# Optimization experiments

Measured on AMD Instinct MI355X. Metric: run time of the kernel, lower is better.

## Reference

```python
import jax, jax.numpy as jnp
import numpy as np

SEM_ENC_DIM = 1024
SENT_HIDDEN_DIM = 1024
ATT_DIM = 512

def setup_inputs() -> dict:
    key = jax.random.key(0)
    ks = jax.random.split(key, 8)
    B, L = 64, 2048
    s = lambda d: 1.0 / np.sqrt(d)
    return {
        "sem_enc_output": jax.random.normal(ks[0], (B, L, SEM_ENC_DIM), dtype=jnp.float32),
        "dec_hidden_state": jax.random.normal(ks[1], (B, SENT_HIDDEN_DIM), dtype=jnp.float32),
        "W_enc": jax.random.uniform(ks[2], (SEM_ENC_DIM, ATT_DIM), jnp.float32, -s(SEM_ENC_DIM), s(SEM_ENC_DIM)),
        "b_enc": jax.random.uniform(ks[3], (ATT_DIM,), jnp.float32, -s(SEM_ENC_DIM), s(SEM_ENC_DIM)),
        "W_dec": jax.random.uniform(ks[4], (SENT_HIDDEN_DIM, ATT_DIM), jnp.float32, -s(SENT_HIDDEN_DIM), s(SENT_HIDDEN_DIM)),
        "b_dec": jax.random.uniform(ks[5], (ATT_DIM,), jnp.float32, -s(SENT_HIDDEN_DIM), s(SENT_HIDDEN_DIM)),
        "W_full": jax.random.uniform(ks[6], (ATT_DIM, 1), jnp.float32, -s(ATT_DIM), s(ATT_DIM)),
        "b_full": jax.random.uniform(ks[7], (1,), jnp.float32, -s(ATT_DIM), s(ATT_DIM)),
    }

def reference(sem_enc_output, dec_hidden_state, W_enc, b_enc, W_dec, b_dec, W_full, b_full):
    # enc projection: [B, L, att_dim]
    enc_proj = jnp.einsum('ble,ea->bla', sem_enc_output, W_enc) + b_enc
    # dec projection: [B, att_dim]
    dec_proj = dec_hidden_state @ W_dec + b_dec
    # broadcast add + tanh: [B, L, att_dim]
    joined = jnp.tanh(enc_proj + dec_proj[:, None, :])
    # scoring: [B, L]
    scores = (jnp.einsum('bla,a->bl', joined, W_full[:, 0]) + b_full[0])
    att_scores = jax.nn.softmax(scores, axis=1)
    # weighted sum over L of the PROJECTED encoder output (matches torch code)
    att_output = jnp.einsum('bl,bla->ba', att_scores, enc_proj)
    return (att_output, att_scores)
```

## Files before the change

### kernel.cpp

```cpp
#include <hip/hip_runtime.h>
#include <hip/hip_bf16.h>
#include <cstdint>
#include <cstddef>

#define BB   64
#define LL   2048
#define ED   1024
#define AD   512
#define BM   64
#define NCH  (LL / BM)
#define KST  32

typedef short  short4v __attribute__((ext_vector_type(4)));
typedef short  short8  __attribute__((ext_vector_type(8)));
typedef float  f32x4   __attribute__((ext_vector_type(4)));

__device__ __forceinline__ unsigned short f2bf(float x) {
  unsigned u = __float_as_uint(x);
  u += 0x7FFFu + ((u >> 16) & 1u);
  return (unsigned short)(u >> 16);
}

__device__ __forceinline__ short4v cvt4(f32x4 v) {
  union { short4v s; unsigned u[2]; } r;
  asm("v_cvt_pk_bf16_f32 %0, %1, %2" : "=v"(r.u[0]) : "v"(v[0]), "v"(v[1]));
  asm("v_cvt_pk_bf16_f32 %0, %1, %2" : "=v"(r.u[1]) : "v"(v[2]), "v"(v[3]));
  return r.s;
}

#define GLOAD_LDS16(gp, lp)                                                        \
  __builtin_amdgcn_global_load_lds(                                                \
      (const __attribute__((address_space(1))) unsigned int*)(gp),                 \
      (__attribute__((address_space(3))) unsigned int*)(lp), 16, 0, 0)

__global__ __launch_bounds__(512) void prep_kernel(
    const float* __restrict__ W_enc, const float* __restrict__ dec,
    const float* __restrict__ W_dec, const float* __restrict__ b_dec,
    unsigned short* __restrict__ Wb, float* __restrict__ dp) {
  const int blk = blockIdx.x, t = threadIdx.x;
  if (blk < BB) {
    const float* drow = dec + blk * ED;
    float a0 = 0.f, a1 = 0.f, a2 = 0.f, a3 = 0.f;
    for (int k = 0; k < ED; k += 4) {
      a0 = fmaf(drow[k],     W_dec[(k)     * AD + t], a0);
      a1 = fmaf(drow[k + 1], W_dec[(k + 1) * AD + t], a1);
      a2 = fmaf(drow[k + 2], W_dec[(k + 2) * AD + t], a2);
      a3 = fmaf(drow[k + 3], W_dec[(k + 3) * AD + t], a3);
    }
    dp[blk * AD + t] = (a0 + a1) + (a2 + a3) + b_dec[t];
  } else {
    const int base = (blk - BB) * 4096;
#pragma unroll
    for (int ii = 0; ii < 8; ii++) {
      const int o    = base + ii * 512 + t;
      const int ks   = o >> 14;
      const int cblk = (o >> 9) & 31;
      const int kg   = (o >> 7) & 3;
      const int r    = (o >> 3) & 15;
      const int j    = o & 7;
      const int k    = ks * 32 + kg * 8 + j;
      const int c    = cblk * 16 + r;
      Wb[o] = f2bf(W_enc[k * AD + c]);
    }
  }
}

__global__ __launch_bounds__(512, 4) void fused_kernel(
    const float* __restrict__ sem, const unsigned short* __restrict__ Wb,
    const float* __restrict__ dp, const float* __restrict__ b_enc,
    const float* __restrict__ Wf,
    float* __restrict__ raw_scores,
    float* __restrict__ ws_ms, float* __restrict__ ws_o) {

  __shared__ unsigned short Ab[2][2048];
  __shared__ unsigned short Bb[2][16384];

  const int t    = threadIdx.x;
  const int lane = t & 63;
  const int wn   = t >> 6;
  const int b    = blockIdx.y;
  const int chunk= blockIdx.x;
  const int l0   = chunk * BM;

  const int srow = t >> 3;
  const int skg  = t & 7;
  const float* aptr = sem + ((size_t)(b * LL + l0 + srow)) * ED + skg * 4;
  const int awr = (srow >> 4) * 512 + (skg >> 1) * 128 + (srow & 15) * 8 + (skg & 1) * 4;

  const unsigned short* bsrc = Wb + t * 8;

  const int arow = lane & 15;
  const int akg  = lane >> 4;
  const int afr  = lane * 8;
  const int bfr  = wn * 2048 + lane * 8;

  f32x4 acc[4][4];
#pragma unroll
  for (int i = 0; i < 4; i++)
#pragma unroll
    for (int j = 0; j < 4; j++) acc[i][j] = (f32x4)0.f;

#pragma unroll
  for (int i = 0; i < 4; i++)
    GLOAD_LDS16(bsrc + i * 4096, &Bb[0][i * 4096 + t * 8]);
  f32x4 pA = *(const f32x4*)(aptr);
  f32x4 qA = *(const f32x4*)(aptr + 32);
  *(short4v*)&Ab[0][awr] = cvt4(pA);
  asm volatile("s_waitcnt vmcnt(1) lgkmcnt(0)" ::: "memory");
  __builtin_amdgcn_sched_barrier(0);
  __builtin_amdgcn_s_barrier();

#define ITER(ks, CA, LA)                                                           \
  {                                                                                \
    const int cb = (ks) & 1, nb = ((ks) + 1) & 1;                                  \
    if ((ks) + 1 < KST) {                                                          \
      const unsigned short* bs = bsrc + ((ks) + 1) * 16384;                        \
      _Pragma("unroll")                                                            \
      for (int i = 0; i < 4; i++)                                                  \
        GLOAD_LDS16(bs + i * 4096, &Bb[nb][i * 4096 + t * 8]);                     \
    }                                                                              \
    __builtin_amdgcn_sched_barrier(0);          \
    if ((ks) + 1 < KST)                                                            \
      *(short4v*)&Ab[nb][awr] = cvt4(CA);          \
    if ((ks) + 2 < KST)                                                            \
      LA = *(const f32x4*)(aptr + ((ks) + 2) * 32);                                \
    short8 av[4], bv[4];                                                           \
    _Pragma("unroll")                                                              \
    for (int mf = 0; mf < 4; mf++)                                                 \
      av[mf] = *(const short8*)&Ab[cb][afr + mf * 512];                            \
    _Pragma("unroll")                                                              \
    for (int nf = 0; nf < 4; nf++)                                                 \
      bv[nf] = *(const short8*)&Bb[cb][bfr + nf * 512];                            \
    __builtin_amdgcn_s_setprio(1);                                                 \
    _Pragma("unroll")                                                              \
    for (int mf = 0; mf < 4; mf++)                                                 \
      _Pragma("unroll")                                                            \
      for (int nf = 0; nf < 4; nf++)                                               \
        acc[mf][nf] = __builtin_amdgcn_mfma_f32_16x16x32_bf16(av[mf], bv[nf], acc[mf][nf], 0, 0, 0); \
    __builtin_amdgcn_s_setprio(0);                                                 \
    if ((ks) + 2 < KST) {                                                          \
      asm volatile("s_waitcnt vmcnt(1) lgkmcnt(0)" ::: "memory");                  \
    } else {                                                                       \
      asm volatile("s_waitcnt vmcnt(0) lgkmcnt(0)" ::: "memory");                  \
    }                                                                              \
    __builtin_amdgcn_sched_barrier(0);                                             \
    __builtin_amdgcn_s_barrier();                                                  \
  }

  for (int kk = 0; kk < KST; kk += 2) {
    ITER(kk,     qA, pA);
    ITER(kk + 1, pA, qA);
  }
#undef ITER

  float* eb = (float*)&Bb[0][0];
  float (*sc_part)[8] = (float (*)[8])eb;
  float* weight       = eb + 512;

  float dpv[4], wfv[4], bev[4];
#pragma unroll
  for (int nf = 0; nf < 4; nf++) {
    const int c = wn * 64 + nf * 16 + arow;
    dpv[nf] = dp[b * AD + c];
    wfv[nf] = Wf[c];
    bev[nf] = b_enc[c];
  }
#pragma unroll
  for (int mf = 0; mf < 4; mf++) {
#pragma unroll
    for (int r = 0; r < 4; r++) {
      float p = 0.f;
#pragma unroll
      for (int nf = 0; nf < 4; nf++) {
        float e = acc[mf][nf][r] + bev[nf];
        acc[mf][nf][r] = e;
        float x = e + dpv[nf];
        float ex = __expf(2.f * x);
        float th = 1.f - 2.f / (ex + 1.f);
        p = fmaf(th, wfv[nf], p);
      }
      p += __shfl_xor(p, 1); p += __shfl_xor(p, 2);
      p += __shfl_xor(p, 4); p += __shfl_xor(p, 8);
      if (arow == 0) sc_part[mf * 16 + akg * 4 + r][wn] = p;
    }
  }
  __syncthreads();

  if (t < BM) {
    float s = sc_part[t][0] + sc_part[t][1] + sc_part[t][2] + sc_part[t][3]
            + sc_part[t][4] + sc_part[t][5] + sc_part[t][6] + sc_part[t][7];
    raw_scores[(size_t)b * LL + l0 + t] = s;
    float m = s;
#pragma unroll
    for (int off = 1; off < 64; off <<= 1) m = fmaxf(m, __shfl_xor(m, off));
    float w = __expf(s - m);
    weight[t] = w;
    float ss = w;
#pragma unroll
    for (int off = 1; off < 64; off <<= 1) ss += __shfl_xor(ss, off);
    if (t == 0) {
      ws_ms[(b * NCH + chunk) * 2]     = m;
      ws_ms[(b * NCH + chunk) * 2 + 1] = ss;
    }
  }
  __syncthreads();

  float wv[4][4];
#pragma unroll
  for (int mf = 0; mf < 4; mf++)
#pragma unroll
    for (int r = 0; r < 4; r++) wv[mf][r] = weight[mf * 16 + akg * 4 + r];
#pragma unroll
  for (int nf = 0; nf < 4; nf++) {
    float cp = 0.f;
#pragma unroll
    for (int mf = 0; mf < 4; mf++)
#pragma unroll
      for (int r = 0; r < 4; r++) cp = fmaf(wv[mf][r], acc[mf][nf][r], cp);
    cp += __shfl_xor(cp, 16);
    cp += __shfl_xor(cp, 32);
    if (lane < 16)
      ws_o[((size_t)b * NCH + chunk) * AD + wn * 64 + nf * 16 + lane] = cp;
  }
}

__global__ __launch_bounds__(256) void finalize_kernel(
    const float* __restrict__ ws_ms, const float* __restrict__ ws_o,
    float* __restrict__ out0, float* __restrict__ outS) {
  const int b = blockIdx.x, t = threadIdx.x;
  float ms[NCH], ss[NCH];
  float M = -1e30f;
#pragma unroll
  for (int i = 0; i < NCH; i++) {
    ms[i] = ws_ms[(b * NCH + i) * 2];
    ss[i] = ws_ms[(b * NCH + i) * 2 + 1];
    M = fmaxf(M, ms[i]);
  }
  float S = 0.f, w[NCH];
#pragma unroll
  for (int i = 0; i < NCH; i++) { w[i] = __expf(ms[i] - M); S = fmaf(ss[i], w[i], S); }
  const float invS = 1.f / S;
  for (int c = t; c < AD; c += 256) {
    float a = 0.f;
#pragma unroll
    for (int i = 0; i < NCH; i++) a = fmaf(ws_o[((size_t)b * NCH + i) * AD + c], w[i], a);
    out0[b * AD + c] = a * invS;
  }
  for (int l = t; l < LL; l += 256) {
    float r = outS[(size_t)b * LL + l];
    outS[(size_t)b * LL + l] = __expf(r - M) * invS;
  }
}

extern "C" void kernel_launch(void* const* d_in, const int* in_sizes, int n_in,
                              void* d_out, int out_size, void* d_ws, size_t ws_size,
                              hipStream_t stream) {
  const float* sem    = (const float*)d_in[0];
  const float* dec    = (const float*)d_in[1];
  const float* W_enc  = (const float*)d_in[2];
  const float* b_enc  = (const float*)d_in[3];
  const float* W_dec  = (const float*)d_in[4];
  const float* b_dec  = (const float*)d_in[5];
  const float* W_full = (const float*)d_in[6];

  float* out0 = (float*)d_out;
  float* outS = out0 + BB * AD;

  char* ws = (char*)d_ws;
  unsigned short* Wb = (unsigned short*)ws;
  float* dpw   = (float*)(ws + (1 << 20));
  float* ws_ms = (float*)(ws + (1 << 20) + (128 << 10));
  float* ws_o  = (float*)(ws + (1 << 20) + (144 << 10));

  prep_kernel<<<BB + 128, 512, 0, stream>>>(W_enc, dec, W_dec, b_dec, Wb, dpw);
  dim3 g1(NCH, BB);
  fused_kernel<<<g1, 512, 0, stream>>>(sem, Wb, dpw, b_enc, W_full, outS, ws_ms, ws_o);
  finalize_kernel<<<BB, 256, 0, stream>>>(ws_ms, ws_o, out0, outS);
}
```

Measured before the change: 278.9 us.

## Restructure decoder projection, widen per-wave GEMM tile, split finalize across blocks

The decoder projection in the prep kernel now stages hidden-state rows through shared memory, so each W_dec load is reused across four batch rows, and it runs in 16 blocks instead of 64. The fused GEMM kernel drops from 512 to 256 threads, each wave now computing a 64x128 output tile with 8 MFMA column fragments, and each thread loads 8 A floats per step. The finalize kernel is split into four blocks per batch row to raise parallelism. The wider tile doubles accumulator registers per thread and halves the waves per block, which may reduce occupancy and latency hiding in the memory-bound stream over the encoder output.

```diff
diff --git a/kernel.cpp b/kernel.cpp
--- a/kernel.cpp
+++ b/kernel.cpp
@@ -38,18 +38,36 @@
     const float* __restrict__ W_dec, const float* __restrict__ b_dec,
     unsigned short* __restrict__ Wb, float* __restrict__ dp) {
   const int blk = blockIdx.x, t = threadIdx.x;
-  if (blk < BB) {
-    const float* drow = dec + blk * ED;
+  if (blk < 16) {
+    __shared__ float ld[64][128];
+    const int cl = t & 31;
+    const int bg = t >> 5;
+    const int c  = blk * 32 + cl;
     float a0 = 0.f, a1 = 0.f, a2 = 0.f, a3 = 0.f;
-    for (int k = 0; k < ED; k += 4) {
-      a0 = fmaf(drow[k],     W_dec[(k)     * AD + t], a0);
-      a1 = fmaf(drow[k + 1], W_dec[(k + 1) * AD + t], a1);
-      a2 = fmaf(drow[k + 2], W_dec[(k + 2) * AD + t], a2);
-      a3 = fmaf(drow[k + 3], W_dec[(k + 3) * AD + t], a3);
+    for (int kc = 0; kc < 8; kc++) {
+      __syncthreads();
+#pragma unroll
+      for (int j = 0; j < 16; j++) {
+        const int idx = j * 512 + t;
+        ld[idx >> 7][idx & 127] = dec[(idx >> 7) * ED + kc * 128 + (idx & 127)];
+      }
+      __syncthreads();
+#pragma unroll 4
+      for (int kk = 0; kk < 128; kk++) {
+        const float w = W_dec[(kc * 128 + kk) * AD + c];
+        a0 = fmaf(ld[bg * 4 + 0][kk], w, a0);
+        a1 = fmaf(ld[bg * 4 + 1][kk], w, a1);
+        a2 = fmaf(ld[bg * 4 + 2][kk], w, a2);
+        a3 = fmaf(ld[bg * 4 + 3][kk], w, a3);
+      }
     }
-    dp[blk * AD + t] = (a0 + a1) + (a2 + a3) + b_dec[t];
+    const float bd = b_dec[c];
+    dp[(bg * 4 + 0) * AD + c] = a0 + bd;
+    dp[(bg * 4 + 1) * AD + c] = a1 + bd;
+    dp[(bg * 4 + 2) * AD + c] = a2 + bd;
+    dp[(bg * 4 + 3) * AD + c] = a3 + bd;
   } else {
-    const int base = (blk - BB) * 4096;
+    const int base = (blk - 16) * 4096;
 #pragma unroll
     for (int ii = 0; ii < 8; ii++) {
       const int o    = base + ii * 512 + t;
@@ -65,15 +83,15 @@
   }
 }
 
-__global__ __launch_bounds__(512, 4) void fused_kernel(
+__global__ __launch_bounds__(256, 2) void fused_kernel(
     const float* __restrict__ sem, const unsigned short* __restrict__ Wb,
     const float* __restrict__ dp, const float* __restrict__ b_enc,
     const float* __restrict__ Wf,
     float* __restrict__ raw_scores,
     float* __restrict__ ws_ms, float* __restrict__ ws_o) {
 
-  __shared__ unsigned short Ab[2][2048];
-  __shared__ unsigned short Bb[2][16384];
+  __shared__ unsigned short Alds[2][2048];
+  __shared__ unsigned short Blds[2][16384];
 
   const int t    = threadIdx.x;
   const int lane = t & 63;
@@ -82,63 +100,80 @@
   const int chunk= blockIdx.x;
   const int l0   = chunk * BM;
 
-  const int srow = t >> 3;
-  const int skg  = t & 7;
-  const float* aptr = sem + ((size_t)(b * LL + l0 + srow)) * ED + skg * 4;
-  const int awr = (srow >> 4) * 512 + (skg >> 1) * 128 + (srow & 15) * 8 + (skg & 1) * 4;
-
+  const int srow = t >> 2;
+  const int skg  = t & 3;
+  const float* aptr = sem + ((size_t)(b * LL + l0 + srow)) * ED + skg * 8;
   const unsigned short* bsrc = Wb + t * 8;
+  const int awr = (srow >> 4) * 512 + skg * 128 + (srow & 15) * 8;
 
   const int arow = lane & 15;
   const int akg  = lane >> 4;
   const int afr  = lane * 8;
-  const int bfr  = wn * 2048 + lane * 8;
-
-  f32x4 acc[4][4];
+  const int bfr  = wn * 4096 + lane * 8;
+
+  f32x4 acc[4][8];
 #pragma unroll
   for (int i = 0; i < 4; i++)
 #pragma unroll
-    for (int j = 0; j < 4; j++) acc[i][j] = (f32x4)0.f;
-
-#pragma unroll
-  for (int i = 0; i < 4; i++)
-    GLOAD_LDS16(bsrc + i * 4096, &Bb[0][i * 4096 + t * 8]);
-  f32x4 pA = *(const f32x4*)(aptr);
-  f32x4 qA = *(const f32x4*)(aptr + 32);
-  *(short4v*)&Ab[0][awr] = cvt4(pA);
-  asm volatile("s_waitcnt vmcnt(1) lgkmcnt(0)" ::: "memory");
+    for (int j = 0; j < 8; j++) acc[i][j] = (f32x4)0.f;
+
+  {
+    f32x4 f0 = *(const f32x4*)(aptr);
+    f32x4 f1 = *(const f32x4*)(aptr + 4);
+#pragma unroll
+    for (int i = 0; i < 8; i++)
+      GLOAD_LDS16(bsrc + i * 2048, &Blds[0][i * 2048 + t * 8]);
+    __builtin_amdgcn_sched_barrier(0);
+    short4v lo = cvt4(f0), hi = cvt4(f1);
+    *(short4v*)&Alds[0][awr]     = lo;
+    *(short4v*)&Alds[0][awr + 4] = hi;
+  }
+  asm volatile("s_waitcnt vmcnt(0) lgkmcnt(0)" ::: "memory");
   __builtin_amdgcn_sched_barrier(0);
   __builtin_amdgcn_s_barrier();
 
-#define ITER(ks, CA, LA)                                                           \
+  f32x4 pA0, pA1, qA0, qA1;
+  {
+    const float* ap = aptr + 32;
+    qA0 = *(const f32x4*)(ap);
+    qA1 = *(const f32x4*)(ap + 4);
+  }
+
+#define ITER(ks, CA0, CA1, LA0, LA1)                                               \
   {                                                                                \
     const int cb = (ks) & 1, nb = ((ks) + 1) & 1;                                  \
     if ((ks) + 1 < KST) {                                                          \
       const unsigned short* bs = bsrc + ((ks) + 1) * 16384;                        \
       _Pragma("unroll")                                                            \
-      for (int i = 0; i < 4; i++)                                                  \
-        GLOAD_LDS16(bs + i * 4096, &Bb[nb][i * 4096 + t * 8]);                     \
+      for (int i = 0; i < 8; i++)                                                  \
+        GLOAD_LDS16(bs + i * 2048, &Blds[nb][i * 2048 + t * 8]);                   \
     }                                                                              \
     __builtin_amdgcn_sched_barrier(0);          \
-    if ((ks) + 1 < KST)                                                            \
-      *(short4v*)&Ab[nb][awr] = cvt4(CA);          \
-    if ((ks) + 2 < KST)                                                            \
-      LA = *(const f32x4*)(aptr + ((ks) + 2) * 32);                                \
-    short8 av[4], bv[4];                                                           \
+    if ((ks) + 1 < KST) {                                                          \
+      short4v lo = cvt4(CA0), hi = cvt4(CA1);                                      \
+      *(short4v*)&Alds[nb][awr]     = lo;                                          \
+      *(short4v*)&Alds[nb][awr + 4] = hi;                                          \
+    }                                                                              \
+    if ((ks) + 2 < KST) {                                                          \
+      const float* ap = aptr + ((ks) + 2) * 32;                                    \
+      LA0 = *(const f32x4*)(ap);                                                   \
+      LA1 = *(const f32x4*)(ap + 4);                                               \
+    }                                                                              \
+    short8 av[4], bv[8];                                                           \
     _Pragma("unroll")                                                              \
     for (int mf = 0; mf < 4; mf++)                                                 \
-      av[mf] = *(const short8*)&Ab[cb][afr + mf * 512];                            \
+      av[mf] = *(const short8*)&Alds[cb][afr + mf * 512];                          \
     _Pragma("unroll")                                                              \
-    for (int nf = 0; nf < 4; nf++)                                                 \
-      bv[nf] = *(const short8*)&Bb[cb][bfr + nf * 512];                            \
+    for (int nf = 0; nf < 8; nf++)                                                 \
+      bv[nf] = *(const short8*)&Blds[cb][bfr + nf * 512];                          \
     __builtin_amdgcn_s_setprio(1);                                                 \
     _Pragma("unroll")                                                              \
     for (int mf = 0; mf < 4; mf++)                                                 \
       _Pragma("unroll")                                                            \
-      for (int nf = 0; nf < 4; nf++)                                               \
+      for (int nf = 0; nf < 8; nf++)                                               \
         acc[mf][nf] = __builtin_amdgcn_mfma_f32_16x16x32_bf16(av[mf], bv[nf], acc[mf][nf], 0, 0, 0); \
     __builtin_amdgcn_s_setprio(0);                                                 \
-    if ((ks) + 2 < KST) {                                                          \
+    if ((ks) + 2 < KST) {   \
       asm volatile("s_waitcnt vmcnt(1) lgkmcnt(0)" ::: "memory");                  \
     } else {                                                                       \
       asm volatile("s_waitcnt vmcnt(0) lgkmcnt(0)" ::: "memory");                  \
@@ -148,19 +183,19 @@
   }
 
   for (int kk = 0; kk < KST; kk += 2) {
-    ITER(kk,     qA, pA);
-    ITER(kk + 1, pA, qA);
+    ITER(kk,     qA0, qA1, pA0, pA1);
+    ITER(kk + 1, pA0, pA1, qA0, qA1);
   }
 #undef ITER
 
-  float* eb = (float*)&Bb[0][0];
-  float (*sc_part)[8] = (float (*)[8])eb;
-  float* weight       = eb + 512;
-
-  float dpv[4], wfv[4], bev[4];
-#pragma unroll
-  for (int nf = 0; nf < 4; nf++) {
-    const int c = wn * 64 + nf * 16 + arow;
+  float* eb = (float*)&Blds[0][0];
+  float (*sc_part)[4] = (float (*)[4])eb;
+  float* weight       = eb + 256;
+
+  float dpv[8], wfv[8], bev[8];
+#pragma unroll
+  for (int nf = 0; nf < 8; nf++) {
+    const int c = wn * 128 + nf * 16 + arow;
     dpv[nf] = dp[b * AD + c];
     wfv[nf] = Wf[c];
     bev[nf] = b_enc[c];
@@ -171,7 +206,7 @@
     for (int r = 0; r < 4; r++) {
       float p = 0.f;
 #pragma unroll
-      for (int nf = 0; nf < 4; nf++) {
+      for (int nf = 0; nf < 8; nf++) {
         float e = acc[mf][nf][r] + bev[nf];
         acc[mf][nf][r] = e;
         float x = e + dpv[nf];
@@ -187,8 +222,7 @@
   __syncthreads();
 
   if (t < BM) {
-    float s = sc_part[t][0] + sc_part[t][1] + sc_part[t][2] + sc_part[t][3]
-            + sc_part[t][4] + sc_part[t][5] + sc_part[t][6] + sc_part[t][7];
+    float s = sc_part[t][0] + sc_part[t][1] + sc_part[t][2] + sc_part[t][3];
     raw_scores[(size_t)b * LL + l0 + t] = s;
     float m = s;
 #pragma unroll
@@ -211,7 +245,7 @@
 #pragma unroll
     for (int r = 0; r < 4; r++) wv[mf][r] = weight[mf * 16 + akg * 4 + r];
 #pragma unroll
-  for (int nf = 0; nf < 4; nf++) {
+  for (int nf = 0; nf < 8; nf++) {
     float cp = 0.f;
 #pragma unroll
     for (int mf = 0; mf < 4; mf++)
@@ -220,16 +254,17 @@
     cp += __shfl_xor(cp, 16);
     cp += __shfl_xor(cp, 32);
     if (lane < 16)
-      ws_o[((size_t)b * NCH + chunk) * AD + wn * 64 + nf * 16 + lane] = cp;
+      ws_o[((size_t)b * NCH + chunk) * AD + wn * 128 + nf * 16 + lane] = cp;
   }
 }
 
 __global__ __launch_bounds__(256) void finalize_kernel(
     const float* __restrict__ ws_ms, const float* __restrict__ ws_o,
     float* __restrict__ out0, float* __restrict__ outS) {
-  const int b = blockIdx.x, t = threadIdx.x;
+  const int blk = blockIdx.x, t = threadIdx.x;
+  const int b = blk >> 2, q = blk & 3;
+  float M = -1e30f;
   float ms[NCH], ss[NCH];
-  float M = -1e30f;
 #pragma unroll
   for (int i = 0; i < NCH; i++) {
     ms[i] = ws_ms[(b * NCH + i) * 2];
@@ -240,13 +275,16 @@
 #pragma unroll
   for (int i = 0; i < NCH; i++) { w[i] = __expf(ms[i] - M); S = fmaf(ss[i], w[i], S); }
   const float invS = 1.f / S;
-  for (int c = t; c < AD; c += 256) {
+  if (t < 128) {
+    const int c = q * 128 + t;
     float a = 0.f;
 #pragma unroll
     for (int i = 0; i < NCH; i++) a = fmaf(ws_o[((size_t)b * NCH + i) * AD + c], w[i], a);
     out0[b * AD + c] = a * invS;
   }
-  for (int l = t; l < LL; l += 256) {
+#pragma unroll
+  for (int j = 0; j < 2; j++) {
+    const int l = q * 512 + j * 256 + t;
     float r = outS[(size_t)b * LL + l];
     outS[(size_t)b * LL + l] = __expf(r - M) * invS;
   }
@@ -272,8 +310,8 @@
   float* ws_ms = (float*)(ws + (1 << 20) + (128 << 10));
   float* ws_o  = (float*)(ws + (1 << 20) + (144 << 10));
 
-  prep_kernel<<<BB + 128, 512, 0, stream>>>(W_enc, dec, W_dec, b_dec, Wb, dpw);
+  prep_kernel<<<144, 512, 0, stream>>>(W_enc, dec, W_dec, b_dec, Wb, dpw);
   dim3 g1(NCH, BB);
-  fused_kernel<<<g1, 512, 0, stream>>>(sem, Wb, dpw, b_enc, W_full, outS, ws_ms, ws_o);
-  finalize_kernel<<<BB, 256, 0, stream>>>(ws_ms, ws_o, out0, outS);
-}
+  fused_kernel<<<g1, 256, 0, stream>>>(sem, Wb, dpw, b_enc, W_full, outS, ws_ms, ws_o);
+  finalize_kernel<<<BB * 4, 256, 0, stream>>>(ws_ms, ws_o, out0, outS);
+}
```

Result: slower. 363.6 us (+30.4%).
